# Kernel optimization log

Hardware: AMD Instinct MI355X
Metric: run time of the kernel (lower is better)

The kernel has to match this reference:

```python
import jax, jax.numpy as jnp
import numpy as np

B, TQ, TI, TT = 8, 256, 256, 256
H, NH, F, E = 1024, 16, 4096, 8
HD = H // NH
EPS = 1e-5


def _ln(x, g, b):
    m = x.mean(-1, keepdims=True)
    v = ((x - m) ** 2).mean(-1, keepdims=True)
    return (x - m) / jnp.sqrt(v + EPS) * g + b


def _mha(q, k, v, in_w, in_b, out_w, out_b):
    # torch nn.MultiheadAttention: packed in_proj [3H,H], out_proj [H,H]
    wq, wk, wv = jnp.split(in_w, 3, axis=0)
    bq, bk, bv = jnp.split(in_b, 3, axis=0)
    Bq, Tq, _ = q.shape
    Tk = k.shape[1]
    qh = (q @ wq.T + bq).reshape(Bq, Tq, NH, HD)
    kh = (k @ wk.T + bk).reshape(Bq, Tk, NH, HD)
    vh = (v @ wv.T + bv).reshape(Bq, Tk, NH, HD)
    scores = jnp.einsum('bqhd,bkhd->bhqk', qh, kh) / jnp.sqrt(jnp.float32(HD))
    attn = jax.nn.softmax(scores, axis=-1)
    out = jnp.einsum('bhqk,bkhd->bqhd', attn, vh).reshape(Bq, Tq, H)
    return out @ out_w.T + out_b


def _moe(x, w1, b1, w2, b2, probs):
    # dense all-expert FFN: GELU(x W1 + b1) W2 + b2, mixed by router probs
    h = jax.nn.gelu(jnp.einsum('bth,ehf->btef', x, w1) + b1, approximate=False)
    o = jnp.einsum('btef,efh->bteh', h, w2) + b2
    return (o * probs[..., None]).sum(axis=-2)


def setup_inputs() -> dict:
    key = jax.random.key(0)
    ks = jax.random.split(key, 24)
    s = 0.02
    d = {}
    d['query_tokens'] = jax.random.normal(ks[0], (B, TQ, H), jnp.float32)
    d['image_tokens'] = jax.random.normal(ks[1], (B, TI, H), jnp.float32)
    d['text_context'] = jax.random.normal(ks[2], (B, TT, H), jnp.float32)
    d['sa_in_w'] = jax.random.normal(ks[3], (3 * H, H), jnp.float32) * s
    d['sa_in_b'] = jnp.zeros((3 * H,), jnp.float32)
    d['sa_out_w'] = jax.random.normal(ks[4], (H, H), jnp.float32) * s
    d['sa_out_b'] = jnp.zeros((H,), jnp.float32)
    d['ca_in_w'] = jax.random.normal(ks[5], (3 * H, H), jnp.float32) * s
    d['ca_in_b'] = jnp.zeros((3 * H,), jnp.float32)
    d['ca_out_w'] = jax.random.normal(ks[6], (H, H), jnp.float32) * s
    d['ca_out_b'] = jnp.zeros((H,), jnp.float32)
    d['img_gate_w'] = jax.random.normal(ks[7], (E, 2 * H), jnp.float32) * s
    d['img_gate_b'] = jnp.zeros((E,), jnp.float32)
    d['txt_gate_w'] = jax.random.normal(ks[8], (E, 2 * H), jnp.float32) * s
    d['txt_gate_b'] = jnp.zeros((E,), jnp.float32)
    d['lnq_g'] = jnp.ones((H,), jnp.float32)
    d['lnq_b'] = jnp.zeros((H,), jnp.float32)
    d['lnc_g'] = jnp.ones((H,), jnp.float32)
    d['lnc_b'] = jnp.zeros((H,), jnp.float32)
    d['lnf_g'] = jnp.ones((H,), jnp.float32)
    d['lnf_b'] = jnp.zeros((H,), jnp.float32)
    d['ew1'] = jax.random.normal(ks[9], (E, H, F), jnp.float32) * s
    d['eb1'] = jnp.zeros((E, F), jnp.float32)
    d['ew2'] = jax.random.normal(ks[10], (E, F, H), jnp.float32) * s
    d['eb2'] = jnp.zeros((E, H), jnp.float32)
    return d


def reference(query_tokens, image_tokens, text_context,
              sa_in_w, sa_in_b, sa_out_w, sa_out_b,
              ca_in_w, ca_in_b, ca_out_w, ca_out_b,
              img_gate_w, img_gate_b, txt_gate_w, txt_gate_b,
              lnq_g, lnq_b, lnc_g, lnc_b, lnf_g, lnf_b,
              ew1, eb1, ew2, eb2):
    # self-attention on query stream (dropout is identity in eval)
    q_norm = _ln(query_tokens, lnq_g, lnq_b)
    query_tokens = query_tokens + _mha(q_norm, q_norm, q_norm, sa_in_w, sa_in_b, sa_out_w, sa_out_b)
    # cross-attention query -> image tokens
    cross_norm = _ln(query_tokens, lnc_g, lnc_b)
    query_tokens = query_tokens + _mha(cross_norm, image_tokens, image_tokens, ca_in_w, ca_in_b, ca_out_w, ca_out_b)
    # gating contexts
    image_ctx = image_tokens.mean(axis=1, keepdims=True)   # [B,1,H]
    text_ctx = text_context.mean(axis=1, keepdims=True)    # [B,1,H]
    img_gate_in = jnp.concatenate([image_tokens, jnp.broadcast_to(text_ctx, image_tokens.shape)], axis=-1)
    txt_gate_in = jnp.concatenate([query_tokens, jnp.broadcast_to(image_ctx, query_tokens.shape)], axis=-1)
    temp = jnp.maximum(jnp.float32(1.0), 0.001)  # router temperature buffer = 1.0
    image_probs = jax.nn.softmax((img_gate_in @ img_gate_w.T + img_gate_b) / temp, axis=-1)
    text_probs = jax.nn.softmax((txt_gate_in @ txt_gate_w.T + txt_gate_b) / temp, axis=-1)
    # dense MoE (ep_group is None -> all experts evaluated, mixed by full softmax)
    q_ffn = _ln(query_tokens, lnf_g, lnf_b)
    query_tokens = query_tokens + _moe(q_ffn, ew1, eb1, ew2, eb2, text_probs)
    image_tokens = image_tokens + _moe(image_tokens, ew1, eb1, ew2, eb2, image_probs)
    return query_tokens, image_tokens
```

## Files before the change

### kernel.cpp

```cpp
#include <hip/hip_runtime.h>
#include <math.h>

typedef unsigned short u16;
typedef __bf16 bf16x8 __attribute__((ext_vector_type(8)));
typedef float  f32x4  __attribute__((ext_vector_type(4)));
typedef unsigned short u16x8 __attribute__((ext_vector_type(8)));
typedef unsigned short u16x4 __attribute__((ext_vector_type(4)));

union B8 { u16x8 u; bf16x8 b; };

__device__ __forceinline__ u16 f2bf(float x) {
  unsigned int u = __float_as_uint(x);
  unsigned int r = (u + 0x7fffu + ((u >> 16) & 1u)) >> 16;
  return (u16)r;
}
__device__ __forceinline__ float bf2f(u16 h) {
  return __uint_as_float(((unsigned int)h) << 16);
}

__device__ __forceinline__ void gload16(const void* g, void* l) {
  __builtin_amdgcn_global_load_lds(
      (const __attribute__((address_space(1))) unsigned int*)g,
      (__attribute__((address_space(3))) unsigned int*)l, 16, 0, 0);
}

__global__ __launch_bounds__(256) void cast_kernel(const float* __restrict__ in,
                                                   u16* __restrict__ out, int n4) {
  int i = blockIdx.x * 256 + threadIdx.x;
  if (i >= n4) return;
  f32x4 v = *(const f32x4*)(in + (size_t)i * 4);
  u16x4 o;
  o[0] = f2bf(v[0]); o[1] = f2bf(v[1]); o[2] = f2bf(v[2]); o[3] = f2bf(v[3]);
  *(u16x4*)(out + (size_t)i * 4) = o;
}

__global__ void transpose_cast_kernel(const float* __restrict__ in, u16* __restrict__ out,
                                      int R, int C) {
  __shared__ float tile[32][33];
  int z = blockIdx.z;
  int r0 = blockIdx.y * 32, c0 = blockIdx.x * 32;
  const float* ip = in + (size_t)z * R * C;
  u16* op = out + (size_t)z * R * C;
  int tx = threadIdx.x, ty = threadIdx.y;
  #pragma unroll
  for (int i = 0; i < 32; i += 8)
    tile[ty + i][tx] = ip[(size_t)(r0 + ty + i) * C + c0 + tx];
  __syncthreads();
  #pragma unroll
  for (int i = 0; i < 32; i += 8)
    op[(size_t)(c0 + ty + i) * R + r0 + tx] = f2bf(tile[tx][ty + i]);
}

__global__ __launch_bounds__(256) void ln_kernel(const float* __restrict__ in,
                                                 const float* __restrict__ g,
                                                 const float* __restrict__ bt,
                                                 u16* __restrict__ out) {
  __shared__ float red[4];
  int row = blockIdx.x;
  int t = threadIdx.x;
  int lane = t & 63, wid = t >> 6;
  f32x4 x = *(const f32x4*)(in + (size_t)row * 1024 + t * 4);
  float s = x[0] + x[1] + x[2] + x[3];
  #pragma unroll
  for (int o = 32; o > 0; o >>= 1) s += __shfl_down(s, o, 64);
  if (lane == 0) red[wid] = s;
  __syncthreads();
  float mean = (red[0] + red[1] + red[2] + red[3]) * (1.0f / 1024.0f);
  __syncthreads();
  float d0 = x[0] - mean, d1 = x[1] - mean, d2 = x[2] - mean, d3 = x[3] - mean;
  float s2 = d0 * d0 + d1 * d1 + d2 * d2 + d3 * d3;
  #pragma unroll
  for (int o = 32; o > 0; o >>= 1) s2 += __shfl_down(s2, o, 64);
  if (lane == 0) red[wid] = s2;
  __syncthreads();
  float var = (red[0] + red[1] + red[2] + red[3]) * (1.0f / 1024.0f);
  float rstd = rsqrtf(var + 1e-5f);
  f32x4 gg = *(const f32x4*)(g + t * 4);
  f32x4 bb = *(const f32x4*)(bt + t * 4);
  u16x4 o;
  o[0] = f2bf(d0 * rstd * gg[0] + bb[0]);
  o[1] = f2bf(d1 * rstd * gg[1] + bb[1]);
  o[2] = f2bf(d2 * rstd * gg[2] + bb[2]);
  o[3] = f2bf(d3 * rstd * gg[3] + bb[3]);
  *(u16x4*)(out + (size_t)row * 1024 + t * 4) = o;
}

__device__ __forceinline__ float gelu_f(float x) {
  float y = 0.79788456080286536f * (x + 0.044715f * x * x * x);
  return x - __fdividef(x, __expf(2.0f * y) + 1.0f);
}

#define SRC_COL(t) ((((t) & 3) ^ (((t) >> 3) & 3)) * 8)

template <int MODE, int ZB, int CHUNK>
__global__ __launch_bounds__(256, 3) void gemm_bt(const u16* __restrict__ A,
                                                  const u16* __restrict__ B,
                                                  const float* __restrict__ bias,
                                                  const float* __restrict__ extra,
                                                  void* __restrict__ out,
                                                  int M, int N, int K, int expertBase,
                                                  int kChunk, size_t saz, size_t sbz,
                                                  int sbiasz, size_t soutz) {
  __shared__ u16 sm[24576];
  const int tid = threadIdx.x;
  const int lane = tid & 63;
  const int wid = tid >> 6;
  const int wr = wid >> 1, wc = wid & 1;
  const int l15 = lane & 15;
  const int kg = lane >> 4;
  const int kgr8 = (kg ^ ((lane >> 1) & 3)) * 8;
  const int z = blockIdx.z;

  const int ze = (ZB == 2) ? (z >> 1) : z;
  if (ZB) { A += (size_t)ze * saz; B += (size_t)ze * sbz; bias += ze * sbiasz; }
  const int kOff = (ZB == 0) ? z * kChunk : (ZB == 2 ? (z & 1) * kChunk : 0);
  const bool z0 = (ZB == 0) ? (z == 0) : (ZB == 1 ? true : ((z & 1) == 0));
  const int expert = expertBase + (ZB ? ze : 0);

  const int gx = gridDim.x, gy = gridDim.y;
  const int bid = blockIdx.y * gx + blockIdx.x;
  const int xcd = bid & 7;
  const int idx = bid >> 3;
  int m0, n0;
  if constexpr (CHUNK == 0) {
    const int nwg = gx * gy;
    const int swz = xcd * (nwg >> 3) + idx;
    m0 = (swz / gx) * 128;
    n0 = (swz % gx) * 128;
  } else {
    const int hy = gy >> 2, hx = gx >> 1;
    const int cy = xcd >> 1, cx = xcd & 1;
    const int mloc = idx % hy;
    const int nloc = idx / hy;
    m0 = (cy * hy + mloc) * 128;
    n0 = (cx * hx + nloc) * 128;
  }

  f32x4 acc[4][4];
  #pragma unroll
  for (int i = 0; i < 4; i++)
    #pragma unroll
    for (int j = 0; j < 4; j++) acc[i][j] = f32x4{0.f, 0.f, 0.f, 0.f};

  const int sc = SRC_COL(tid);
  const u16* ga = A + (size_t)(m0 + (tid >> 2)) * K + sc + kOff;
  const u16* gb = B + (size_t)(n0 + (tid >> 2)) * K + sc + kOff;
  const size_t rowskip = (size_t)64 * K;

#define STG(b, kt)                                                  \
  do {                                                              \
    u16* d = sm + (b) * 8192 + wid * 512;                           \
    gload16(ga + (kt), d);                                          \
    gload16(ga + rowskip + (kt), d + 2048);                         \
    gload16(gb + (kt), d + 4096);                                   \
    gload16(gb + rowskip + (kt), d + 6144);                         \
  } while (0)

  const int NT = kChunk >> 5;
  STG(0, 0); STG(1, 32);
  int buf = 0;
  for (int t = 0; t < NT; ++t) {
    if (t + 1 < NT) asm volatile("s_waitcnt vmcnt(4)" ::: "memory");
    else            asm volatile("s_waitcnt vmcnt(0)" ::: "memory");
    __builtin_amdgcn_s_barrier();
    if (t + 2 < NT) {
      int nb = buf + 2; if (nb >= 3) nb -= 3;
      STG(nb, (t + 2) * 32);
    }
    __builtin_amdgcn_sched_barrier(0);
    __builtin_amdgcn_s_setprio(1);
    const u16* base = sm + buf * 8192;
    B8 af[4], bfr[4];
    #pragma unroll
    for (int i = 0; i < 4; i++) {
      af[i].u  = *(const u16x8*)(base + (wr * 64 + l15 + i * 16) * 32 + kgr8);
      bfr[i].u = *(const u16x8*)(base + 4096 + (wc * 64 + l15 + i * 16) * 32 + kgr8);
    }
    #pragma unroll
    for (int i = 0; i < 4; i++)
      #pragma unroll
      for (int j = 0; j < 4; j++)
        acc[i][j] = __builtin_amdgcn_mfma_f32_16x16x32_bf16(af[i].b, bfr[j].b, acc[i][j], 0, 0, 0);
    __builtin_amdgcn_s_setprio(0);
    if (++buf >= 3) buf = 0;
  }
#undef STG

  const int orow0 = m0 + wr * 64 + (lane >> 4) * 4;
  const int ocol0 = n0 + wc * 64 + l15;

  if constexpr (MODE == 0 || MODE == 2) {
    u16* outp = (u16*)out + (ZB ? (size_t)ze * soutz : 0);
    __builtin_amdgcn_s_barrier();
    u16* rp = sm + wid * 1152;
    const int mrow0 = m0 + wr * 64;
    const int cbase = n0 + wc * 64;
    #pragma unroll
    for (int i = 0; i < 4; i++) {
      #pragma unroll
      for (int j = 0; j < 4; j++) {
        const float bb = bias[cbase + j * 16 + l15];
        #pragma unroll
        for (int p = 0; p < 4; p++) {
          float vb = acc[i][j][p] + bb;
          if constexpr (MODE == 2) vb = gelu_f(vb);
          rp[((lane >> 4) * 4 + p) * 72 + j * 16 + l15] = f2bf(vb);
        }
      }
      asm volatile("s_waitcnt lgkmcnt(0)" ::: "memory");
      #pragma unroll
      for (int rr = 0; rr < 4; rr++) {
        const int r16 = rr * 4 + (lane >> 4);
        u16x4 v4 = *(const u16x4*)&rp[r16 * 72 + l15 * 4];
        *(u16x4*)(outp + (size_t)(mrow0 + i * 16 + r16) * N + cbase + l15 * 4) = v4;
      }
      asm volatile("s_waitcnt lgkmcnt(0)" ::: "memory");
    }
  } else {
    float* outp = (float*)out + (ZB ? (size_t)ze * soutz : 0);
    #pragma unroll
    for (int i = 0; i < 4; i++) {
      float pr_[4];
      if constexpr (MODE == 3) {
        #pragma unroll
        for (int p = 0; p < 4; p++)
          pr_[p] = extra[(size_t)(orow0 + i * 16 + p) * 8 + expert];
      }
      #pragma unroll
      for (int j = 0; j < 4; j++) {
        const int gcol = ocol0 + j * 16;
        const float bb = bias[gcol];
        #pragma unroll
        for (int p = 0; p < 4; p++) {
          const int grow = orow0 + i * 16 + p;
          const size_t off = (size_t)grow * N + gcol;
          if constexpr (MODE == 1) {
            atomicAdd(&outp[off], acc[i][j][p] + (z0 ? bb + extra[off] : 0.f));
          } else {
            atomicAdd(&outp[off], pr_[p] * (acc[i][j][p] + (z0 ? bb : 0.f)));
          }
        }
      }
    }
  }
}

__global__ __launch_bounds__(256, 2) void gemm_w1(const u16* __restrict__ A,
                                                  const u16* __restrict__ B,
                                                  const float* __restrict__ bias,
                                                  u16* __restrict__ out,
                                                  int N, int K,
                                                  size_t sbz, int sbiasz, size_t soutz) {
  __shared__ u16 sm[36864];
  const int tid = threadIdx.x;
  const int lane = tid & 63;
  const int wid = tid >> 6;
  const int wr = wid >> 1, wc = wid & 1;
  const int l15 = lane & 15;
  const int kg = lane >> 4;
  const int kgr8 = (kg ^ ((lane >> 1) & 3)) * 8;
  const int z = blockIdx.z;
  B += (size_t)z * sbz; bias += z * sbiasz;
  u16* outp = out + (size_t)z * soutz;

  const int gx = gridDim.x, gy = gridDim.y;
  const int bid = blockIdx.y * gx + blockIdx.x;
  const int xcd = bid & 7;
  const int idx = bid >> 3;
  const int hy = gy >> 2, hx = gx >> 1;
  const int cy = xcd >> 1, cx = xcd & 1;
  const int m0 = (cy * hy + idx % hy) * 256;
  const int n0 = (cx * hx + idx / hy) * 128;

  f32x4 acc[8][4];
  #pragma unroll
  for (int i = 0; i < 8; i++)
    #pragma unroll
    for (int j = 0; j < 4; j++) acc[i][j] = f32x4{0.f, 0.f, 0.f, 0.f};

  const int sc = SRC_COL(tid);
  const u16* ga = A + (size_t)(m0 + (tid >> 2)) * K + sc;
  const u16* gb = B + (size_t)(n0 + (tid >> 2)) * K + sc;
  const size_t r64 = (size_t)64 * K;

#define STGW(b, kt)                                                 \
  do {                                                              \
    u16* d = sm + (b) * 12288 + wid * 512;                          \
    gload16(ga + (kt), d);                                          \
    gload16(ga + r64 + (kt), d + 2048);                             \
    gload16(ga + 2 * r64 + (kt), d + 4096);                         \
    gload16(ga + 3 * r64 + (kt), d + 6144);                         \
    gload16(gb + (kt), d + 8192);                                   \
    gload16(gb + r64 + (kt), d + 10240);                            \
  } while (0)

  const int NT = K >> 5;
  STGW(0, 0); STGW(1, 32);
  int buf = 0;
  for (int t = 0; t < NT; ++t) {
    if (t + 1 < NT) asm volatile("s_waitcnt vmcnt(6)" ::: "memory");
    else            asm volatile("s_waitcnt vmcnt(0)" ::: "memory");
    __builtin_amdgcn_s_barrier();
    if (t + 2 < NT) {
      int nb = buf + 2; if (nb >= 3) nb -= 3;
      STGW(nb, (t + 2) * 32);
    }
    __builtin_amdgcn_sched_barrier(0);
    __builtin_amdgcn_s_setprio(1);
    const u16* base = sm + buf * 12288;
    B8 af[8], bfr[4];
    #pragma unroll
    for (int j = 0; j < 4; j++)
      bfr[j].u = *(const u16x8*)(base + 8192 + (wc * 64 + j * 16 + l15) * 32 + kgr8);
    #pragma unroll
    for (int i = 0; i < 8; i++)
      af[i].u = *(const u16x8*)(base + (wr * 128 + i * 16 + l15) * 32 + kgr8);
    #pragma unroll
    for (int i = 0; i < 8; i++)
      #pragma unroll
      for (int j = 0; j < 4; j++)
        acc[i][j] = __builtin_amdgcn_mfma_f32_16x16x32_bf16(af[i].b, bfr[j].b, acc[i][j], 0, 0, 0);
    __builtin_amdgcn_s_setprio(0);
    if (++buf >= 3) buf = 0;
  }
#undef STGW

  __builtin_amdgcn_s_barrier();
  u16* rp = sm + wid * 1152;
  const int mrow0 = m0 + wr * 128;
  const int cbase = n0 + wc * 64;
  #pragma unroll
  for (int i = 0; i < 8; i++) {
    #pragma unroll
    for (int j = 0; j < 4; j++) {
      const float bb = bias[cbase + j * 16 + l15];
      #pragma unroll
      for (int p = 0; p < 4; p++) {
        float vb = gelu_f(acc[i][j][p] + bb);
        rp[((lane >> 4) * 4 + p) * 72 + j * 16 + l15] = f2bf(vb);
      }
    }
    asm volatile("s_waitcnt lgkmcnt(0)" ::: "memory");
    #pragma unroll
    for (int rr = 0; rr < 4; rr++) {
      const int r16 = rr * 4 + (lane >> 4);
      u16x4 v4 = *(const u16x4*)&rp[r16 * 72 + l15 * 4];
      *(u16x4*)(outp + (size_t)(mrow0 + i * 16 + r16) * N + cbase + l15 * 4) = v4;
    }
    asm volatile("s_waitcnt lgkmcnt(0)" ::: "memory");
  }
}

__global__ __launch_bounds__(256) void attn_mfma(const u16* __restrict__ qb, int qs,
                                                 const u16* __restrict__ kb_, int ks,
                                                 const u16* __restrict__ vb, int vs,
                                                 u16* __restrict__ outp) {
  __shared__ u16 Ks[64][72];
  __shared__ u16 Vt[64][72];
  __shared__ u16 Pl[4][64][72];
  const int t = threadIdx.x;
  const int lane = t & 63;
  const int w = t >> 6;
  const int b = blockIdx.x >> 4;
  const int h = blockIdx.x & 15;
  const int lr = lane & 15;
  const int kg = lane >> 4;
  const size_t qrow0 = (size_t)b * 256 + w * 64;

  B8 qf[4][2];
  #pragma unroll
  for (int i = 0; i < 4; i++)
    #pragma unroll
    for (int kk = 0; kk < 2; kk++)
      qf[i][kk].u = *(const u16x8*)(qb + (qrow0 + i * 16 + lr) * qs + h * 64 + kk * 32 + kg * 8);

  f32x4 ao[4][4];
  float m_[4][4], l_[4][4];
  #pragma unroll
  for (int i = 0; i < 4; i++)
    #pragma unroll
    for (int n = 0; n < 4; n++) ao[i][n] = f32x4{0.f, 0.f, 0.f, 0.f};
  #pragma unroll
  for (int i = 0; i < 4; i++)
    #pragma unroll
    for (int p = 0; p < 4; p++) { m_[i][p] = -1e30f; l_[i][p] = 0.f; }

  for (int jt = 0; jt < 4; ++jt) {
    __syncthreads();
    {
      int r = t >> 2, c = (t & 3) * 16;
      const u16* src = kb_ + ((size_t)b * 256 + jt * 64 + r) * ks + h * 64 + c;
      *(u16x8*)&Ks[r][c] = *(const u16x8*)src;
      *(u16x8*)&Ks[r][c + 8] = *(const u16x8*)(src + 8);
      int jj = t & 63;
      const u16* vsrc = vb + ((size_t)b * 256 + jt * 64 + jj) * vs + h * 64 + w * 16;
      u16x8 v0 = *(const u16x8*)vsrc;
      u16x8 v1 = *(const u16x8*)(vsrc + 8);
      #pragma unroll
      for (int d = 0; d < 8; d++) Vt[w * 16 + d][jj] = v0[d];
      #pragma unroll
      for (int d = 0; d < 8; d++) Vt[w * 16 + 8 + d][jj] = v1[d];
    }
    __syncthreads();

    B8 kf[2][4];
    #pragma unroll
    for (int kk = 0; kk < 2; kk++)
      #pragma unroll
      for (int n = 0; n < 4; n++)
        kf[kk][n].u = *(const u16x8*)&Ks[n * 16 + lr][kk * 32 + kg * 8];

    #pragma unroll
    for (int i = 0; i < 4; i++) {
      f32x4 s[4];
      #pragma unroll
      for (int n = 0; n < 4; n++) s[n] = f32x4{0.f, 0.f, 0.f, 0.f};
      #pragma unroll
      for (int kk = 0; kk < 2; kk++)
        #pragma unroll
        for (int n = 0; n < 4; n++)
          s[n] = __builtin_amdgcn_mfma_f32_16x16x32_bf16(qf[i][kk].b, kf[kk][n].b, s[n], 0, 0, 0);
      #pragma unroll
      for (int p = 0; p < 4; p++) {
        float pm = fmaxf(fmaxf(s[0][p], s[1][p]), fmaxf(s[2][p], s[3][p])) * 0.125f;
        #pragma unroll
        for (int mk = 1; mk < 16; mk <<= 1) pm = fmaxf(pm, __shfl_xor(pm, mk, 16));
        float mn = fmaxf(m_[i][p], pm);
        float scl = __expf(m_[i][p] - mn);
        m_[i][p] = mn;
        float rs = 0.f;
        #pragma unroll
        for (int n = 0; n < 4; n++) {
          float e = __expf(s[n][p] * 0.125f - mn);
          Pl[w][i * 16 + kg * 4 + p][n * 16 + lr] = f2bf(e);
          rs += e;
        }
        #pragma unroll
        for (int mk = 1; mk < 16; mk <<= 1) rs += __shfl_xor(rs, mk, 16);
        l_[i][p] = l_[i][p] * scl + rs;
        #pragma unroll
        for (int n2 = 0; n2 < 4; n2++) ao[i][n2][p] *= scl;
      }
    }

    B8 vf[2][4];
    #pragma unroll
    for (int kk = 0; kk < 2; kk++)
      #pragma unroll
      for (int n2 = 0; n2 < 4; n2++)
        vf[kk][n2].u = *(const u16x8*)&Vt[n2 * 16 + lr][kk * 32 + kg * 8];
    #pragma unroll
    for (int i = 0; i < 4; i++) {
      #pragma unroll
      for (int kk = 0; kk < 2; kk++) {
        B8 pa;
        pa.u = *(const u16x8*)&Pl[w][i * 16 + lr][kk * 32 + kg * 8];
        #pragma unroll
        for (int n2 = 0; n2 < 4; n2++)
          ao[i][n2] = __builtin_amdgcn_mfma_f32_16x16x32_bf16(pa.b, vf[kk][n2].b, ao[i][n2], 0, 0, 0);
      }
    }
  }

  #pragma unroll
  for (int i = 0; i < 4; i++) {
    #pragma unroll
    for (int p = 0; p < 4; p++) {
      const float inv = 1.0f / l_[i][p];
      const size_t row = qrow0 + i * 16 + kg * 4 + p;
      #pragma unroll
      for (int n2 = 0; n2 < 4; n2++)
        outp[row * 1024 + h * 64 + n2 * 16 + lr] = f2bf(ao[i][n2][p] * inv);
    }
  }
}

__global__ __launch_bounds__(256) void mean2_kernel(const float* __restrict__ in,
                                                    float* __restrict__ out) {
  __shared__ float part[128];
  const int blk = blockIdx.x;
  const int b = blk >> 3, ch = blk & 7;
  const int t = threadIdx.x;
  const int col = ch * 128 + (t & 127);
  const int half = t >> 7;
  const float* p = in + (size_t)b * 262144 + (size_t)half * 131072 + col;
  float s = 0.f;
  for (int r = 0; r < 128; r++) s += p[(size_t)r * 1024];
  if (half) part[t & 127] = s;
  __syncthreads();
  if (!half) out[b * 1024 + col] = (s + part[t & 127]) * (1.0f / 256.0f);
}

__global__ __launch_bounds__(256) void gate_kernel(const float* __restrict__ x,
                                                   const float* __restrict__ ctx,
                                                   const float* __restrict__ gw,
                                                   const float* __restrict__ gb,
                                                   float* __restrict__ probs, int rowoff) {
  __shared__ float lg[8];
  const int tok = blockIdx.x;
  const int b = tok >> 8;
  const int t = threadIdx.x;
  const int e = t >> 5, sl = t & 31;
  const float* xr = x + (size_t)tok * 1024;
  const float* cr = ctx + (size_t)b * 1024;
  const float* wrow = gw + (size_t)e * 2048;
  float s = 0.f;
  for (int c = sl; c < 1024; c += 32) s += xr[c] * wrow[c] + cr[c] * wrow[1024 + c];
  #pragma unroll
  for (int o = 16; o > 0; o >>= 1) s += __shfl_down(s, o, 32);
  if (sl == 0) lg[e] = s + gb[e];
  __syncthreads();
  if (t == 0) {
    float mx = lg[0];
    #pragma unroll
    for (int i = 1; i < 8; i++) mx = fmaxf(mx, lg[i]);
    float ex[8], sum = 0.f;
    #pragma unroll
    for (int i = 0; i < 8; i++) { ex[i] = expf(lg[i] - mx); sum += ex[i]; }
    float inv = 1.0f / sum;
    #pragma unroll
    for (int i = 0; i < 8; i++) probs[(size_t)(rowoff + tok) * 8 + i] = ex[i] * inv;
  }
}

__global__ __launch_bounds__(256) void final_add_kernel(const float* __restrict__ q3,
                                                        const float* __restrict__ img,
                                                        const float* __restrict__ moe,
                                                        float* __restrict__ out) {
  size_t i = (size_t)blockIdx.x * 256 + threadIdx.x;
  f32x4 m4 = *(const f32x4*)(moe + i * 4);
  f32x4 a4 = (i < 524288) ? *(const f32x4*)(q3 + i * 4)
                          : *(const f32x4*)(img + (i - 524288) * 4);
  f32x4 r;
  r[0] = a4[0] + m4[0]; r[1] = a4[1] + m4[1]; r[2] = a4[2] + m4[2]; r[3] = a4[3] + m4[3];
  *(f32x4*)(out + i * 4) = r;
}

extern "C" void kernel_launch(void* const* d_in, const int* in_sizes, int n_in,
                              void* d_out, int out_size, void* d_ws, size_t ws_size,
                              hipStream_t stream) {
  const float* query_in = (const float*)d_in[0];
  const float* image_in = (const float*)d_in[1];
  const float* text_in  = (const float*)d_in[2];
  const float* sa_in_w  = (const float*)d_in[3];
  const float* sa_in_b  = (const float*)d_in[4];
  const float* sa_out_w = (const float*)d_in[5];
  const float* sa_out_b = (const float*)d_in[6];
  const float* ca_in_w  = (const float*)d_in[7];
  const float* ca_in_b  = (const float*)d_in[8];
  const float* ca_out_w = (const float*)d_in[9];
  const float* ca_out_b = (const float*)d_in[10];
  const float* img_gate_w = (const float*)d_in[11];
  const float* img_gate_b = (const float*)d_in[12];
  const float* txt_gate_w = (const float*)d_in[13];
  const float* txt_gate_b = (const float*)d_in[14];
  const float* lnq_g = (const float*)d_in[15];
  const float* lnq_b = (const float*)d_in[16];
  const float* lnc_g = (const float*)d_in[17];
  const float* lnc_b = (const float*)d_in[18];
  const float* lnf_g = (const float*)d_in[19];
  const float* lnf_b = (const float*)d_in[20];
  const float* ew1 = (const float*)d_in[21];
  const float* eb1 = (const float*)d_in[22];
  const float* ew2 = (const float*)d_in[23];
  const float* eb2 = (const float*)d_in[24];

  char* base = (char*)d_ws;
  size_t off = 0;
  auto alloc = [&](size_t bytes) -> char* {
    char* p = base + off;
    off += (bytes + 255) & ~(size_t)255;
    return p;
  };

  u16* wsa_in  = (u16*)alloc((size_t)3072 * 1024 * 2);
  u16* wsa_out = (u16*)alloc((size_t)1024 * 1024 * 2);
  u16* wca_in  = (u16*)alloc((size_t)3072 * 1024 * 2);
  u16* wca_out = (u16*)alloc((size_t)1024 * 1024 * 2);
  u16* w1T = (u16*)alloc((size_t)8 * 4096 * 1024 * 2);
  u16* w2T = (u16*)alloc((size_t)8 * 4096 * 1024 * 2);
  char* big = alloc((size_t)67108864);
  float* q3 = (float*)alloc((size_t)2048 * 1024 * 4);
  u16* xmoe = (u16*)alloc((size_t)4096 * 1024 * 2);
  float* moeac = (float*)alloc((size_t)4096 * 1024 * 4);
  float* probs = (float*)alloc((size_t)4096 * 8 * 4);
  float* ctx = (float*)alloc((size_t)2 * 8192 * 4);

  u16* qn      = (u16*)big;
  u16* qkv     = (u16*)(big + 4194304);
  u16* attn_o  = (u16*)(big + 16777216);
  float* q2    = (float*)(big + 20971520);
  u16* cnorm   = (u16*)(big + 29360128);
  u16* qca     = (u16*)(big + 33554432);
  u16* kvca    = (u16*)(big + 37748736);
  u16* h1p     = (u16*)big;
  u16* img_bf  = xmoe + (size_t)2048 * 1024;

  cast_kernel<<<3072, 256, 0, stream>>>(sa_in_w, wsa_in, 786432);
  cast_kernel<<<1024, 256, 0, stream>>>(sa_out_w, wsa_out, 262144);
  cast_kernel<<<3072, 256, 0, stream>>>(ca_in_w, wca_in, 786432);
  cast_kernel<<<1024, 256, 0, stream>>>(ca_out_w, wca_out, 262144);
  transpose_cast_kernel<<<dim3(128, 32, 8), dim3(32, 8), 0, stream>>>(ew1, w1T, 1024, 4096);
  transpose_cast_kernel<<<dim3(32, 128, 8), dim3(32, 8), 0, stream>>>(ew2, w2T, 4096, 1024);
  cast_kernel<<<2048, 256, 0, stream>>>(image_in, img_bf, 524288);

  ln_kernel<<<2048, 256, 0, stream>>>(query_in, lnq_g, lnq_b, qn);
  gemm_bt<0, 0, 0><<<dim3(24, 16), 256, 0, stream>>>(qn, wsa_in, sa_in_b, nullptr, qkv,
                                                     2048, 3072, 1024, 0, 1024, 0, 0, 0, 0);
  attn_mfma<<<128, 256, 0, stream>>>(qkv, 3072, qkv + 1024, 3072, qkv + 2048, 3072, attn_o);
  hipMemsetAsync(q2, 0, (size_t)2048 * 1024 * 4, stream);
  gemm_bt<1, 0, 0><<<dim3(8, 16, 2), 256, 0, stream>>>(attn_o, wsa_out, sa_out_b, query_in, q2,
                                                       2048, 1024, 1024, 0, 512, 0, 0, 0, 0);

  ln_kernel<<<2048, 256, 0, stream>>>(q2, lnc_g, lnc_b, cnorm);
  gemm_bt<0, 0, 0><<<dim3(8, 16), 256, 0, stream>>>(cnorm, wca_in, ca_in_b, nullptr, qca,
                                                    2048, 1024, 1024, 0, 1024, 0, 0, 0, 0);
  gemm_bt<0, 0, 0><<<dim3(16, 16), 256, 0, stream>>>(img_bf, wca_in + (size_t)1024 * 1024,
                                                     ca_in_b + 1024, nullptr, kvca,
                                                     2048, 2048, 1024, 0, 1024, 0, 0, 0, 0);
  attn_mfma<<<128, 256, 0, stream>>>(qca, 1024, kvca, 2048, kvca + 1024, 2048, attn_o);
  hipMemsetAsync(q3, 0, (size_t)2048 * 1024 * 4, stream);
  gemm_bt<1, 0, 0><<<dim3(8, 16, 2), 256, 0, stream>>>(attn_o, wca_out, ca_out_b, q2, q3,
                                                       2048, 1024, 1024, 0, 512, 0, 0, 0, 0);

  mean2_kernel<<<64, 256, 0, stream>>>(image_in, ctx);
  mean2_kernel<<<64, 256, 0, stream>>>(text_in, ctx + 8192);
  gate_kernel<<<2048, 256, 0, stream>>>(q3, ctx, txt_gate_w, txt_gate_b, probs, 0);
  gate_kernel<<<2048, 256, 0, stream>>>(image_in, ctx + 8192, img_gate_w, img_gate_b, probs, 2048);

  ln_kernel<<<2048, 256, 0, stream>>>(q3, lnf_g, lnf_b, xmoe);
  hipMemsetAsync(moeac, 0, (size_t)4096 * 1024 * 4, stream);
  for (int e0 = 0; e0 < 8; e0 += 2) {
    gemm_w1<<<dim3(32, 16, 2), 256, 0, stream>>>(
        xmoe, w1T + (size_t)e0 * 4194304, eb1 + (size_t)e0 * 4096, h1p,
        4096, 1024,  4194304,  4096,  16777216);
    gemm_bt<3, 2, 0><<<dim3(8, 32, 4), 256, 0, stream>>>(
        h1p, w2T + (size_t)e0 * 4194304, eb2 + (size_t)e0 * 1024, probs, moeac,
        4096, 1024, 4096, e0, 2048,
         16777216,  4194304,  1024,  0);
  }

  final_add_kernel<<<4096, 256, 0, stream>>>(q3, image_in, moeac, (float*)d_out);
}
```

Baseline: 1.163 ms.

## Use 256x256 eight-wave tiles for MoE W1 GEMM, drop split-K in W2

The MoE up-projection kernel now uses 512-thread blocks computing 256x256 output tiles. It runs a 4-stage LDS ring with staggered A/B loads interleaved between two MFMA halves, and the grid halves in x. The W2 down-projection no longer splits K across two z-slices per expert, so each block covers the full K=4096 and there are half as many atomic adds. The intent is more data reuse per block and less atomic traffic, at the cost of more LDS per block, lower occupancy and fewer blocks to fill the GPU.

```diff
diff --git a/kernel.cpp b/kernel.cpp
--- a/kernel.cpp
+++ b/kernel.cpp
@@ -111,11 +111,10 @@
   const int kgr8 = (kg ^ ((lane >> 1) & 3)) * 8;
   const int z = blockIdx.z;
 
-  const int ze = (ZB == 2) ? (z >> 1) : z;
-  if (ZB) { A += (size_t)ze * saz; B += (size_t)ze * sbz; bias += ze * sbiasz; }
-  const int kOff = (ZB == 0) ? z * kChunk : (ZB == 2 ? (z & 1) * kChunk : 0);
-  const bool z0 = (ZB == 0) ? (z == 0) : (ZB == 1 ? true : ((z & 1) == 0));
-  const int expert = expertBase + (ZB ? ze : 0);
+  if (ZB) { A += (size_t)z * saz; B += (size_t)z * sbz; bias += z * sbiasz; }
+  const int kOff = ZB ? 0 : z * kChunk;
+  const bool z0 = ZB ? true : (z == 0);
+  const int expert = expertBase + (ZB ? z : 0);
 
   const int gx = gridDim.x, gy = gridDim.y;
   const int bid = blockIdx.y * gx + blockIdx.x;
@@ -130,10 +129,8 @@
   } else {
     const int hy = gy >> 2, hx = gx >> 1;
     const int cy = xcd >> 1, cx = xcd & 1;
-    const int mloc = idx % hy;
-    const int nloc = idx / hy;
-    m0 = (cy * hy + mloc) * 128;
-    n0 = (cx * hx + nloc) * 128;
+    m0 = (cy * hy + idx % hy) * 128;
+    n0 = (cx * hx + idx / hy) * 128;
   }
 
   f32x4 acc[4][4];
@@ -190,7 +187,7 @@
   const int ocol0 = n0 + wc * 64 + l15;
 
   if constexpr (MODE == 0 || MODE == 2) {
-    u16* outp = (u16*)out + (ZB ? (size_t)ze * soutz : 0);
+    u16* outp = (u16*)out + (ZB ? (size_t)z * soutz : 0);
     __builtin_amdgcn_s_barrier();
     u16* rp = sm + wid * 1152;
     const int mrow0 = m0 + wr * 64;
@@ -217,7 +214,7 @@
       asm volatile("s_waitcnt lgkmcnt(0)" ::: "memory");
     }
   } else {
-    float* outp = (float*)out + (ZB ? (size_t)ze * soutz : 0);
+    float* outp = (float*)out + (ZB ? (size_t)z * soutz : 0);
     #pragma unroll
     for (int i = 0; i < 4; i++) {
       float pr_[4];
@@ -237,7 +234,7 @@
           if constexpr (MODE == 1) {
             atomicAdd(&outp[off], acc[i][j][p] + (z0 ? bb + extra[off] : 0.f));
           } else {
-            atomicAdd(&outp[off], pr_[p] * (acc[i][j][p] + (z0 ? bb : 0.f)));
+            atomicAdd(&outp[off], pr_[p] * (acc[i][j][p] + bb));
           }
         }
       }
@@ -245,17 +242,18 @@
   }
 }
 
-__global__ __launch_bounds__(256, 2) void gemm_w1(const u16* __restrict__ A,
-                                                  const u16* __restrict__ B,
-                                                  const float* __restrict__ bias,
-                                                  u16* __restrict__ out,
-                                                  int N, int K,
-                                                  size_t sbz, int sbiasz, size_t soutz) {
-  __shared__ u16 sm[36864];
+__global__ __launch_bounds__(512, 2) void gemm8p(const u16* __restrict__ A,
+                                                 const u16* __restrict__ B,
+                                                 const float* __restrict__ bias,
+                                                 u16* __restrict__ out,
+                                                 int N, int K,
+                                                 size_t sbz, int sbiasz, size_t soutz) {
+  __shared__ u16 sm[65536];
   const int tid = threadIdx.x;
   const int lane = tid & 63;
   const int wid = tid >> 6;
-  const int wr = wid >> 1, wc = wid & 1;
+  const int wr = wid >> 2;
+  const int wc = wid & 3;
   const int l15 = lane & 15;
   const int kg = lane >> 4;
   const int kgr8 = (kg ^ ((lane >> 1) & 3)) * 8;
@@ -270,7 +268,7 @@
   const int hy = gy >> 2, hx = gx >> 1;
   const int cy = xcd >> 1, cx = xcd & 1;
   const int m0 = (cy * hy + idx % hy) * 256;
-  const int n0 = (cx * hx + idx / hy) * 128;
+  const int n0 = (cx * hx + idx / hy) * 256;
 
   f32x4 acc[8][4];
   #pragma unroll
@@ -279,51 +277,73 @@
     for (int j = 0; j < 4; j++) acc[i][j] = f32x4{0.f, 0.f, 0.f, 0.f};
 
   const int sc = SRC_COL(tid);
-  const u16* ga = A + (size_t)(m0 + (tid >> 2)) * K + sc;
-  const u16* gb = B + (size_t)(n0 + (tid >> 2)) * K + sc;
-  const size_t r64 = (size_t)64 * K;
-
-#define STGW(b, kt)                                                 \
+  const u16* gaA0 = A + (size_t)(m0 + (tid >> 2)) * K + sc;
+  const u16* gaA1 = A + (size_t)(m0 + 128 + (tid >> 2)) * K + sc;
+  const u16* gbB0 = B + (size_t)(n0 + (tid >> 2)) * K + sc;
+  const u16* gbB1 = B + (size_t)(n0 + 128 + (tid >> 2)) * K + sc;
+
+#define STG_A(sp)                                                   \
   do {                                                              \
-    u16* d = sm + (b) * 12288 + wid * 512;                          \
-    gload16(ga + (kt), d);                                          \
-    gload16(ga + r64 + (kt), d + 2048);                             \
-    gload16(ga + 2 * r64 + (kt), d + 4096);                         \
-    gload16(ga + 3 * r64 + (kt), d + 6144);                         \
-    gload16(gb + (kt), d + 8192);                                   \
-    gload16(gb + r64 + (kt), d + 10240);                            \
+    u16* d = sm + ((sp) & 3) * 8192 + wid * 512;                    \
+    gload16(gaA0 + (size_t)(sp) * 32, d);                           \
+    gload16(gaA1 + (size_t)(sp) * 32, d + 4096);                    \
   } while (0)
+#define STG_B(sp)                                                   \
+  do {                                                              \
+    u16* d = sm + 32768 + ((sp) & 3) * 8192 + wid * 512;            \
+    gload16(gbB0 + (size_t)(sp) * 32, d);                           \
+    gload16(gbB1 + (size_t)(sp) * 32, d + 4096);                    \
+  } while (0)
 
   const int NT = K >> 5;
-  STGW(0, 0); STGW(1, 32);
-  int buf = 0;
-  for (int t = 0; t < NT; ++t) {
-    if (t + 1 < NT) asm volatile("s_waitcnt vmcnt(6)" ::: "memory");
-    else            asm volatile("s_waitcnt vmcnt(0)" ::: "memory");
+  STG_A(0); STG_B(0); STG_A(1); STG_B(1); STG_A(2); STG_B(2);
+  asm volatile("s_waitcnt vmcnt(8)" ::: "memory");
+  __builtin_amdgcn_s_barrier();
+
+  for (int s = 0; s < NT; ++s) {
+    const u16* bA = sm + (s & 3) * 8192;
+    const u16* bB = sm + 32768 + (s & 3) * 8192;
+    B8 bfr[4], af[4];
+    #pragma unroll
+    for (int j = 0; j < 4; j++)
+      bfr[j].u = *(const u16x8*)(bB + (wc * 64 + j * 16 + l15) * 32 + kgr8);
+    #pragma unroll
+    for (int i = 0; i < 4; i++)
+      af[i].u = *(const u16x8*)(bA + (wr * 128 + i * 16 + l15) * 32 + kgr8);
+    if (s + 3 < NT) STG_A(s + 3);
     __builtin_amdgcn_s_barrier();
-    if (t + 2 < NT) {
-      int nb = buf + 2; if (nb >= 3) nb -= 3;
-      STGW(nb, (t + 2) * 32);
-    }
+    asm volatile("s_waitcnt lgkmcnt(0)" ::: "memory");
     __builtin_amdgcn_sched_barrier(0);
     __builtin_amdgcn_s_setprio(1);
-    const u16* base = sm + buf * 12288;
-    B8 af[8], bfr[4];
-    #pragma unroll
-    for (int j = 0; j < 4; j++)
-      bfr[j].u = *(const u16x8*)(base + 8192 + (wc * 64 + j * 16 + l15) * 32 + kgr8);
-    #pragma unroll
-    for (int i = 0; i < 8; i++)
-      af[i].u = *(const u16x8*)(base + (wr * 128 + i * 16 + l15) * 32 + kgr8);
-    #pragma unroll
-    for (int i = 0; i < 8; i++)
+    #pragma unroll
+    for (int i = 0; i < 4; i++)
       #pragma unroll
       for (int j = 0; j < 4; j++)
         acc[i][j] = __builtin_amdgcn_mfma_f32_16x16x32_bf16(af[i].b, bfr[j].b, acc[i][j], 0, 0, 0);
     __builtin_amdgcn_s_setprio(0);
-    if (++buf >= 3) buf = 0;
-  }
-#undef STGW
+    __builtin_amdgcn_s_barrier();
+    B8 af2[4];
+    #pragma unroll
+    for (int i = 0; i < 4; i++)
+      af2[i].u = *(const u16x8*)(bA + (wr * 128 + (i + 4) * 16 + l15) * 32 + kgr8);
+    if (s + 3 < NT) STG_B(s + 3);
+    __builtin_amdgcn_s_barrier();
+    asm volatile("s_waitcnt lgkmcnt(0)" ::: "memory");
+    __builtin_amdgcn_sched_barrier(0);
+    __builtin_amdgcn_s_setprio(1);
+    #pragma unroll
+    for (int i = 0; i < 4; i++)
+      #pragma unroll
+      for (int j = 0; j < 4; j++)
+        acc[i + 4][j] = __builtin_amdgcn_mfma_f32_16x16x32_bf16(af2[i].b, bfr[j].b, acc[i + 4][j], 0, 0, 0);
+    __builtin_amdgcn_s_setprio(0);
+    if (s + 3 < NT)      asm volatile("s_waitcnt vmcnt(8)" ::: "memory");
+    else if (s + 2 < NT) asm volatile("s_waitcnt vmcnt(4)" ::: "memory");
+    else                 asm volatile("s_waitcnt vmcnt(0)" ::: "memory");
+    __builtin_amdgcn_s_barrier();
+  }
+#undef STG_A
+#undef STG_B
 
   __builtin_amdgcn_s_barrier();
   u16* rp = sm + wid * 1152;
@@ -631,12 +651,12 @@
   ln_kernel<<<2048, 256, 0, stream>>>(q3, lnf_g, lnf_b, xmoe);
   hipMemsetAsync(moeac, 0, (size_t)4096 * 1024 * 4, stream);
   for (int e0 = 0; e0 < 8; e0 += 2) {
-    gemm_w1<<<dim3(32, 16, 2), 256, 0, stream>>>(
+    gemm8p<<<dim3(16, 16, 2), 512, 0, stream>>>(
         xmoe, w1T + (size_t)e0 * 4194304, eb1 + (size_t)e0 * 4096, h1p,
         4096, 1024,  4194304,  4096,  16777216);
-    gemm_bt<3, 2, 0><<<dim3(8, 32, 4), 256, 0, stream>>>(
+    gemm_bt<3, 1, 0><<<dim3(8, 32, 2), 256, 0, stream>>>(
         h1p, w2T + (size_t)e0 * 4194304, eb2 + (size_t)e0 * 1024, probs, moeac,
-        4096, 1024, 4096, e0, 2048,
+        4096, 1024, 4096, e0, 4096,
          16777216,  4194304,  1024,  0);
   }
 
```

After: 1.125 ms (median of 3 runs). -3.3%, faster.
